# Kernel optimization log

Hardware: AMD Instinct MI355X
Metric: run time of the kernel (lower is better)

The kernel has to match this reference:

```python
import jax, jax.numpy as jnp
import numpy as np

V, D, H, B, M, T, PAD = 32000, 512, 3, 32, 512, 4, 1


def setup_inputs() -> dict:
    key = jax.random.key(0)
    ks = jax.random.split(key, 10)
    def emb_tables(k):
        t = 0.1 * jax.random.normal(k, (H + 1, V, D), jnp.float32)
        return t.at[:, PAD, :].set(0.0)  # padding_idx rows are zero
    C_enc = emb_tables(ks[0])
    C_dec = emb_tables(ks[1])
    gru_w_ih = 0.1 * jax.random.normal(ks[2], (3 * D, D), jnp.float32)
    gru_w_hh = 0.1 * jax.random.normal(ks[3], (3 * D, D), jnp.float32)
    gru_b_ih = jnp.zeros((3 * D,), jnp.float32)
    gru_b_hh = jnp.zeros((3 * D,), jnp.float32)
    W1_w = 0.1 * jax.random.normal(ks[4], (V, 2 * D), jnp.float32)
    W1_b = jnp.zeros((V,), jnp.float32)
    story = jax.random.randint(ks[5], (B, M, T), 0, V, jnp.int32)
    enc_query = jax.random.randint(ks[6], (B,), 0, V, jnp.int32)
    return {"story": story, "enc_query": enc_query, "C_enc": C_enc,
            "C_dec": C_dec, "gru_w_ih": gru_w_ih, "gru_w_hh": gru_w_hh,
            "gru_b_ih": gru_b_ih, "gru_b_hh": gru_b_hh, "W1_w": W1_w,
            "W1_b": W1_b}


def _mem_embed(table, story):
    # table [V, D], story [B, M, T] -> sum-pooled memory [B, M, D]
    return jnp.sum(table[story], axis=2)


def _forward(C_enc, C_dec, gru_w_ih, gru_w_hh, gru_b_ih, gru_b_hh,
             W1_w, W1_b, story, enc_query):
    # ---- EncoderMemNN.forward (eval mode, no unk_mask dropout) ----
    u = jnp.zeros((story.shape[0], D), C_enc.dtype)
    for hop in range(H):
        m_A = _mem_embed(C_enc[hop], story)            # [B, M, D]
        prob = jax.nn.softmax(jnp.einsum('bmd,bd->bm', m_A, u), axis=1)
        m_C = _mem_embed(C_enc[hop + 1], story)        # [B, M, D]
        u = u + jnp.einsum('bmd,bm->bd', m_C, prob)
    enc_hidden = u                                     # decoder_hidden[0]

    # ---- DecoderrMemNN.ptrMemDecoder: single GRU step ----
    x = C_dec[0][enc_query]                            # [B, D]
    gi = x @ gru_w_ih.T + gru_b_ih                     # [B, 3D]
    gh = enc_hidden @ gru_w_hh.T + gru_b_hh            # [B, 3D]
    i_r, i_z, i_n = jnp.split(gi, 3, axis=1)
    h_r, h_z, h_n = jnp.split(gh, 3, axis=1)
    r = jax.nn.sigmoid(i_r + h_r)
    z = jax.nn.sigmoid(i_z + h_z)
    n = jnp.tanh(i_n + r * h_n)
    hidden = (1.0 - z) * n + z * enc_hidden            # new GRU hidden [B, D]

    # ---- DecoderrMemNN.load_memory: m_story[h] = sum-pooled C_dec[h] ----
    m_story = [_mem_embed(C_dec[h], story) for h in range(H + 1)]

    # ---- multi-hop pointer attention ----
    u0 = hidden
    uk = hidden
    p_vocab = None
    for hop in range(H):
        prob_lg = jnp.einsum('bmd,bd->bm', m_story[hop], uk)   # [B, M]
        prob = jax.nn.softmax(prob_lg, axis=1)
        o_k = jnp.einsum('bmd,bm->bd', m_story[hop + 1], prob)  # [B, D]
        if hop == 0:
            p_vocab = jnp.concatenate([u0, o_k], axis=1) @ W1_w.T + W1_b
        uk = uk + o_k
    p_ptr = prob_lg                                    # logits from last hop
    return p_ptr, p_vocab, hidden[None]                # hidden [1, B, D]


def reference(story, enc_query, C_enc, C_dec, gru_w_ih, gru_w_hh,
              gru_b_ih, gru_b_hh, W1_w, W1_b):
    return _forward(C_enc, C_dec, gru_w_ih, gru_w_hh, gru_b_ih, gru_b_hh,
                    W1_w, W1_b, story, enc_query)
```

## Files before the change

kernel.cpp:

```cpp
#include <hip/hip_runtime.h>
#include <math.h>

#define DD 512
#define MM 512
#define BB 32
#define TT 4
#define VV 32000
#define BMD ((size_t)BB * MM * DD)

__global__ __launch_bounds__(256) void mega_pool(const float* __restrict__ C_enc,
                                                 const float* __restrict__ C_dec,
                                                 const int* __restrict__ story,
                                                 float* __restrict__ P) {
  int g = blockIdx.x;
  int tbl = g >> 12;
  int blk = g & 4095;
  int wave = (blk << 2) + (threadIdx.x >> 6);
  int lane = threadIdx.x & 63;
  const size_t VD = (size_t)VV * DD;
  const float* table = (tbl < 3) ? (C_enc + (size_t)(tbl + 1) * VD)
                                 : (C_dec + (size_t)(tbl - 3) * VD);
  const int* st = story + wave * TT;
  size_t r0 = (size_t)st[0] * DD, r1 = (size_t)st[1] * DD;
  size_t r2 = (size_t)st[2] * DD, r3 = (size_t)st[3] * DD;
  const float4* t4 = (const float4*)table;
  float4* p4 = (float4*)(P + (size_t)tbl * BMD + (size_t)wave * DD);
#pragma unroll
  for (int h = 0; h < 2; ++h) {
    int c = (h << 6) + lane;
    float4 a = t4[(r0 >> 2) + c];
    float4 b = t4[(r1 >> 2) + c];
    float4 cc = t4[(r2 >> 2) + c];
    float4 d = t4[(r3 >> 2) + c];
    float4 r;
    r.x = a.x + b.x + cc.x + d.x;
    r.y = a.y + b.y + cc.y + d.y;
    r.z = a.z + b.z + cc.z + d.z;
    r.w = a.w + b.w + cc.w + d.w;
    p4[c] = r;
  }
}

__global__ __launch_bounds__(256) void wsumA_kernel(const float* __restrict__ P,
                                                    const float* __restrict__ s,
                                                    float* __restrict__ partial) {
  __shared__ float wsh[MM];
  __shared__ float red[16];
  int b = blockIdx.x >> 3;
  int c = blockIdx.x & 7;
  int t = threadIdx.x;
  if (s) {
    float v0 = s[b * MM + t], v1 = s[b * MM + t + 256];
    float mx = fmaxf(v0, v1);
#pragma unroll
    for (int off = 32; off > 0; off >>= 1) mx = fmaxf(mx, __shfl_xor(mx, off));
    if ((t & 63) == 0) red[t >> 6] = mx;
    __syncthreads();
    mx = fmaxf(fmaxf(red[0], red[1]), fmaxf(red[2], red[3]));
    float e0 = expf(v0 - mx), e1 = expf(v1 - mx);
    float sm = e0 + e1;
#pragma unroll
    for (int off = 32; off > 0; off >>= 1) sm += __shfl_xor(sm, off);
    if ((t & 63) == 0) red[8 + (t >> 6)] = sm;
    __syncthreads();
    sm = red[8] + red[9] + red[10] + red[11];
    float inv = 1.0f / sm;
    wsh[t] = e0 * inv;
    wsh[t + 256] = e1 * inv;
    __syncthreads();
  }
  const float* Pb = P + ((size_t)b * MM + c * 64) * DD;
  float acc0 = 0.f, acc1 = 0.f;
  if (s) {
#pragma unroll 8
    for (int m = 0; m < 64; ++m) {
      float wm = wsh[c * 64 + m];
      acc0 += wm * Pb[m * DD + t];
      acc1 += wm * Pb[m * DD + t + 256];
    }
  } else {
#pragma unroll 8
    for (int m = 0; m < 64; ++m) {
      acc0 += Pb[m * DD + t];
      acc1 += Pb[m * DD + t + 256];
    }
    acc0 *= (1.0f / MM);
    acc1 *= (1.0f / MM);
  }
  float* pp = partial + (size_t)blockIdx.x * DD;
  pp[t] = acc0;
  pp[t + 256] = acc1;
}

__global__ void wsumB_kernel(const float* __restrict__ partial,
                             const float* __restrict__ prev,
                             float* __restrict__ uout) {
  int i = blockIdx.x * 256 + threadIdx.x;
  int b = i >> 9, d = i & 511;
  float acc = prev ? prev[i] : 0.f;
  const float* pp = partial + (size_t)b * 8 * DD + d;
#pragma unroll
  for (int c = 0; c < 8; ++c) acc += pp[c * DD];
  uout[i] = acc;
}

__global__ void wsumB2_kernel(const float* __restrict__ partial,
                              const float* __restrict__ hid,
                              float* __restrict__ uk, float* __restrict__ hc) {
  int i = blockIdx.x * 256 + threadIdx.x;
  int b = i >> 9, d = i & 511;
  float ov = 0.f;
  const float* pp = partial + (size_t)b * 8 * DD + d;
#pragma unroll
  for (int c = 0; c < 8; ++c) ov += pp[c * DD];
  float hv = hid[i];
  uk[i] = hv + ov;
  hc[b * 1024 + d] = hv;
  hc[b * 1024 + 512 + d] = ov;
}

__global__ __launch_bounds__(256) void dot_kernel(const float* __restrict__ P,
                                                  const float* __restrict__ u,
                                                  float* __restrict__ s) {
  int p = (blockIdx.x << 2) + (threadIdx.x >> 6);
  int lane = threadIdx.x & 63;
  int b = p >> 9;
  const float4* Pr = (const float4*)(P + (size_t)p * DD);
  const float4* ur = (const float4*)(u + (size_t)b * DD);
  float acc = 0.f;
#pragma unroll
  for (int h = 0; h < 2; ++h) {
    int c = (h << 6) + lane;
    float4 a = Pr[c];
    float4 q = ur[c];
    acc += a.x * q.x + a.y * q.y + a.z * q.z + a.w * q.w;
  }
#pragma unroll
  for (int off = 32; off > 0; off >>= 1) acc += __shfl_xor(acc, off);
  if (lane == 0) s[p] = acc;
}

__global__ __launch_bounds__(256) void matvec_kernel(const float* __restrict__ W,
                                                     const float* __restrict__ bias,
                                                     const float* __restrict__ vin,
                                                     const int* __restrict__ q,
                                                     const float* __restrict__ table,
                                                     float* __restrict__ out) {
  int idx = (blockIdx.x << 2) + (threadIdx.x >> 6);
  int lane = threadIdx.x & 63;
  int b = idx / 1536;
  int j = idx - b * 1536;
  const float* xb = vin ? (vin + (size_t)b * DD) : (table + (size_t)q[b] * DD);
  const float4* Wr = (const float4*)(W + (size_t)j * DD);
  const float4* xr = (const float4*)xb;
  float acc = 0.f;
#pragma unroll
  for (int h = 0; h < 2; ++h) {
    int c = (h << 6) + lane;
    float4 a = Wr[c];
    float4 qv = xr[c];
    acc += a.x * qv.x + a.y * qv.y + a.z * qv.z + a.w * qv.w;
  }
#pragma unroll
  for (int off = 32; off > 0; off >>= 1) acc += __shfl_xor(acc, off);
  if (lane == 0) out[idx] = acc + bias[j];
}

__global__ void gate_kernel(const float* __restrict__ gi, const float* __restrict__ gh,
                            const float* __restrict__ u, float* __restrict__ hidden,
                            float* __restrict__ out_h) {
  int i = blockIdx.x * 256 + threadIdx.x;
  int b = i >> 9, d = i & 511;
  const float* gib = gi + b * 1536;
  const float* ghb = gh + b * 1536;
  float i_r = gib[d], i_z = gib[d + 512], i_n = gib[d + 1024];
  float h_r = ghb[d], h_z = ghb[d + 512], h_n = ghb[d + 1024];
  float r = 1.f / (1.f + expf(-(i_r + h_r)));
  float z = 1.f / (1.f + expf(-(i_z + h_z)));
  float n = tanhf(i_n + r * h_n);
  float h = (1.f - z) * n + z * u[i];
  hidden[i] = h;
  out_h[i] = h;
}

__global__ __launch_bounds__(256) void pvocab_kernel(const float* __restrict__ Hcat,
                                                     const float* __restrict__ W1,
                                                     const float* __restrict__ W1b,
                                                     float* __restrict__ out) {
  __shared__ float As[32][36];
  __shared__ float Bs[32][68];
  int t = threadIdx.x;
  int v0 = blockIdx.x * 64;
  int tb = t >> 5;
  int tv = t & 31;
  int br = t >> 2;
  int bk = (t & 3) << 3;
  const float* Wp = W1 + (size_t)(v0 + br) * 1024 + bk;
  int ab = t >> 3;
  int ak = (t & 7) << 2;
  const float* Ap = Hcat + (size_t)ab * 1024 + ak;

  float acc[4][2] = {{0.f, 0.f}, {0.f, 0.f}, {0.f, 0.f}, {0.f, 0.f}};

  float4 aReg = *(const float4*)(Ap);
  float4 wReg0 = *(const float4*)(Wp);
  float4 wReg1 = *(const float4*)(Wp + 4);

  for (int k0 = 0; k0 < 1024; k0 += 32) {
    As[ak + 0][ab] = aReg.x; As[ak + 1][ab] = aReg.y;
    As[ak + 2][ab] = aReg.z; As[ak + 3][ab] = aReg.w;
    Bs[bk + 0][br] = wReg0.x; Bs[bk + 1][br] = wReg0.y;
    Bs[bk + 2][br] = wReg0.z; Bs[bk + 3][br] = wReg0.w;
    Bs[bk + 4][br] = wReg1.x; Bs[bk + 5][br] = wReg1.y;
    Bs[bk + 6][br] = wReg1.z; Bs[bk + 7][br] = wReg1.w;
    __syncthreads();
    if (k0 + 32 < 1024) {
      aReg = *(const float4*)(Ap + k0 + 32);
      wReg0 = *(const float4*)(Wp + k0 + 32);
      wReg1 = *(const float4*)(Wp + k0 + 36);
    }
#pragma unroll
    for (int k = 0; k < 32; ++k) {
      float2 bv = *(const float2*)&Bs[k][tv * 2];
      float4 av = *(const float4*)&As[k][tb * 4];
      acc[0][0] += av.x * bv.x; acc[0][1] += av.x * bv.y;
      acc[1][0] += av.y * bv.x; acc[1][1] += av.y * bv.y;
      acc[2][0] += av.z * bv.x; acc[2][1] += av.z * bv.y;
      acc[3][0] += av.w * bv.x; acc[3][1] += av.w * bv.y;
    }
    __syncthreads();
  }
  int v = v0 + tv * 2;
  float b0 = W1b[v], b1 = W1b[v + 1];
#pragma unroll
  for (int i = 0; i < 4; ++i) {
    float2 r;
    r.x = acc[i][0] + b0;
    r.y = acc[i][1] + b1;
    *(float2*)(out + (size_t)(tb * 4 + i) * VV + v) = r;
  }
}

extern "C" void kernel_launch(void* const* d_in, const int* in_sizes, int n_in,
                              void* d_out, int out_size, void* d_ws, size_t ws_size,
                              hipStream_t stream) {
  const int* story = (const int*)d_in[0];
  const int* q = (const int*)d_in[1];
  const float* C_enc = (const float*)d_in[2];
  const float* C_dec = (const float*)d_in[3];
  const float* W_ih = (const float*)d_in[4];
  const float* W_hh = (const float*)d_in[5];
  const float* b_ih = (const float*)d_in[6];
  const float* b_hh = (const float*)d_in[7];
  const float* W1 = (const float*)d_in[8];
  const float* W1b = (const float*)d_in[9];
  float* out = (float*)d_out;

  float* P = (float*)d_ws;
  float* u = P + 6 * BMD;
  float* s = u + BB * DD;
  float* part = s + BB * MM;
  float* gi = part + BB * 8 * DD;
  float* gh = gi + BB * 3 * DD;
  float* hid = gh + BB * 3 * DD;
  float* uk = hid + BB * DD;
  float* hc = uk + BB * DD;

  const float* P0 = P;
  const float* P1 = P + 1 * BMD;
  const float* P2 = P + 2 * BMD;
  const float* P3 = P + 3 * BMD;
  const float* P4 = P + 4 * BMD;
  const float* P5 = P + 5 * BMD;

  float* p_ptr_out = out;
  float* p_vocab_out = out + BB * MM;
  float* hid_out = out + BB * MM + (size_t)BB * VV;

  dim3 blk(256);
  const int dotGrid = BB * MM / 4;
  const int mvGrid = BB * 3 * DD / 4;
  const int ewGrid = BB * DD / 256;

  mega_pool<<<6 * 4096, blk, 0, stream>>>(C_enc, C_dec, story, P);

  wsumA_kernel<<<BB * 8, blk, 0, stream>>>(P0, nullptr, part);
  wsumB_kernel<<<ewGrid, blk, 0, stream>>>(part, nullptr, u);
  dot_kernel<<<dotGrid, blk, 0, stream>>>(P0, u, s);
  wsumA_kernel<<<BB * 8, blk, 0, stream>>>(P1, s, part);
  wsumB_kernel<<<ewGrid, blk, 0, stream>>>(part, u, u);
  dot_kernel<<<dotGrid, blk, 0, stream>>>(P1, u, s);
  wsumA_kernel<<<BB * 8, blk, 0, stream>>>(P2, s, part);
  wsumB_kernel<<<ewGrid, blk, 0, stream>>>(part, u, u);

  matvec_kernel<<<mvGrid, blk, 0, stream>>>(W_ih, b_ih, nullptr, q, C_dec, gi);
  matvec_kernel<<<mvGrid, blk, 0, stream>>>(W_hh, b_hh, u, nullptr, nullptr, gh);
  gate_kernel<<<ewGrid, blk, 0, stream>>>(gi, gh, u, hid, hid_out);

  dot_kernel<<<dotGrid, blk, 0, stream>>>(P3, hid, s);
  wsumA_kernel<<<BB * 8, blk, 0, stream>>>(P4, s, part);
  wsumB2_kernel<<<ewGrid, blk, 0, stream>>>(part, hid, uk, hc);
  dot_kernel<<<dotGrid, blk, 0, stream>>>(P4, uk, s);
  wsumA_kernel<<<BB * 8, blk, 0, stream>>>(P5, s, part);
  wsumB_kernel<<<ewGrid, blk, 0, stream>>>(part, uk, uk);
  dot_kernel<<<dotGrid, blk, 0, stream>>>(P5, uk, p_ptr_out);

  pvocab_kernel<<<VV / 64, blk, 0, stream>>>(hc, W1, W1b, p_vocab_out);
}
```

Measured before the change: 314.2 us.

## Fuse embedding gather-pooling into attention dot and weighted-sum kernels

Removes the upfront pooling kernel that materialized six pooled memory tensors in workspace, and instead gathers and sums embedding rows on the fly inside the dot-product and weighted-sum kernels. The weighted-sum kernel now splits each batch into 32 chunks of 16 memory slots, so the partial reductions sum over 32 partials. This avoids writing and re-reading about 200MB of pooled intermediates. In exchange each table is gathered twice (once for dot, once for weighted sum), with random-row access patterns.

```diff
diff --git a/kernel.cpp b/kernel.cpp
--- a/kernel.cpp
+++ b/kernel.cpp
@@ -6,48 +6,16 @@
 #define BB 32
 #define TT 4
 #define VV 32000
-#define BMD ((size_t)BB * MM * DD)
-
-__global__ __launch_bounds__(256) void mega_pool(const float* __restrict__ C_enc,
-                                                 const float* __restrict__ C_dec,
-                                                 const int* __restrict__ story,
-                                                 float* __restrict__ P) {
-  int g = blockIdx.x;
-  int tbl = g >> 12;
-  int blk = g & 4095;
-  int wave = (blk << 2) + (threadIdx.x >> 6);
-  int lane = threadIdx.x & 63;
-  const size_t VD = (size_t)VV * DD;
-  const float* table = (tbl < 3) ? (C_enc + (size_t)(tbl + 1) * VD)
-                                 : (C_dec + (size_t)(tbl - 3) * VD);
-  const int* st = story + wave * TT;
-  size_t r0 = (size_t)st[0] * DD, r1 = (size_t)st[1] * DD;
-  size_t r2 = (size_t)st[2] * DD, r3 = (size_t)st[3] * DD;
-  const float4* t4 = (const float4*)table;
-  float4* p4 = (float4*)(P + (size_t)tbl * BMD + (size_t)wave * DD);
-#pragma unroll
-  for (int h = 0; h < 2; ++h) {
-    int c = (h << 6) + lane;
-    float4 a = t4[(r0 >> 2) + c];
-    float4 b = t4[(r1 >> 2) + c];
-    float4 cc = t4[(r2 >> 2) + c];
-    float4 d = t4[(r3 >> 2) + c];
-    float4 r;
-    r.x = a.x + b.x + cc.x + d.x;
-    r.y = a.y + b.y + cc.y + d.y;
-    r.z = a.z + b.z + cc.z + d.z;
-    r.w = a.w + b.w + cc.w + d.w;
-    p4[c] = r;
-  }
-}
-
-__global__ __launch_bounds__(256) void wsumA_kernel(const float* __restrict__ P,
-                                                    const float* __restrict__ s,
-                                                    float* __restrict__ partial) {
-  __shared__ float wsh[MM];
+
+__global__ __launch_bounds__(256) void poolwsum_kernel(const float* __restrict__ table,
+                                                       const int* __restrict__ story,
+                                                       const float* __restrict__ s,
+                                                       float* __restrict__ partial) {
+  __shared__ float wsh[16];
+  __shared__ int rows[64];
   __shared__ float red[16];
-  int b = blockIdx.x >> 3;
-  int c = blockIdx.x & 7;
+  int b = blockIdx.x >> 5;
+  int c = blockIdx.x & 31;
   int t = threadIdx.x;
   if (s) {
     float v0 = s[b * MM + t], v1 = s[b * MM + t + 256];
@@ -65,27 +33,19 @@
     __syncthreads();
     sm = red[8] + red[9] + red[10] + red[11];
     float inv = 1.0f / sm;
-    wsh[t] = e0 * inv;
-    wsh[t + 256] = e1 * inv;
-    __syncthreads();
-  }
-  const float* Pb = P + ((size_t)b * MM + c * 64) * DD;
+    if (t < 16) wsh[t] = expf(s[b * MM + c * 16 + t] - mx) * inv;
+  } else {
+    if (t < 16) wsh[t] = 1.0f / MM;
+  }
+  if (t < 64) rows[t] = story[((b << 9) + (c << 4)) * TT + t];
+  __syncthreads();
   float acc0 = 0.f, acc1 = 0.f;
-  if (s) {
 #pragma unroll 8
-    for (int m = 0; m < 64; ++m) {
-      float wm = wsh[c * 64 + m];
-      acc0 += wm * Pb[m * DD + t];
-      acc1 += wm * Pb[m * DD + t + 256];
-    }
-  } else {
-#pragma unroll 8
-    for (int m = 0; m < 64; ++m) {
-      acc0 += Pb[m * DD + t];
-      acc1 += Pb[m * DD + t + 256];
-    }
-    acc0 *= (1.0f / MM);
-    acc1 *= (1.0f / MM);
+  for (int i = 0; i < 64; ++i) {
+    const float* r = table + (size_t)rows[i] * DD;
+    float wm = wsh[i >> 2];
+    acc0 += wm * r[t];
+    acc1 += wm * r[t + 256];
   }
   float* pp = partial + (size_t)blockIdx.x * DD;
   pp[t] = acc0;
@@ -98,9 +58,9 @@
   int i = blockIdx.x * 256 + threadIdx.x;
   int b = i >> 9, d = i & 511;
   float acc = prev ? prev[i] : 0.f;
-  const float* pp = partial + (size_t)b * 8 * DD + d;
-#pragma unroll
-  for (int c = 0; c < 8; ++c) acc += pp[c * DD];
+  const float* pp = partial + (size_t)b * 32 * DD + d;
+#pragma unroll
+  for (int c = 0; c < 32; ++c) acc += pp[c * DD];
   uout[i] = acc;
 }
 
@@ -110,34 +70,44 @@
   int i = blockIdx.x * 256 + threadIdx.x;
   int b = i >> 9, d = i & 511;
   float ov = 0.f;
-  const float* pp = partial + (size_t)b * 8 * DD + d;
-#pragma unroll
-  for (int c = 0; c < 8; ++c) ov += pp[c * DD];
+  const float* pp = partial + (size_t)b * 32 * DD + d;
+#pragma unroll
+  for (int c = 0; c < 32; ++c) ov += pp[c * DD];
   float hv = hid[i];
   uk[i] = hv + ov;
   hc[b * 1024 + d] = hv;
   hc[b * 1024 + 512 + d] = ov;
 }
 
-__global__ __launch_bounds__(256) void dot_kernel(const float* __restrict__ P,
-                                                  const float* __restrict__ u,
-                                                  float* __restrict__ s) {
-  int p = (blockIdx.x << 2) + (threadIdx.x >> 6);
+__global__ __launch_bounds__(256) void pooldot_kernel(const float* __restrict__ table,
+                                                      const int* __restrict__ story,
+                                                      const float* __restrict__ u,
+                                                      float* __restrict__ s) {
+  int wave = (blockIdx.x << 2) + (threadIdx.x >> 6);
   int lane = threadIdx.x & 63;
-  int b = p >> 9;
-  const float4* Pr = (const float4*)(P + (size_t)p * DD);
+  int b = wave >> 9;
+  const int* st = story + wave * TT;
+  size_t r0 = (size_t)st[0] * DD, r1 = (size_t)st[1] * DD;
+  size_t r2 = (size_t)st[2] * DD, r3 = (size_t)st[3] * DD;
+  const float4* t4 = (const float4*)table;
   const float4* ur = (const float4*)(u + (size_t)b * DD);
   float acc = 0.f;
 #pragma unroll
   for (int h = 0; h < 2; ++h) {
     int c = (h << 6) + lane;
-    float4 a = Pr[c];
+    float4 a = t4[(r0 >> 2) + c];
+    float4 bb = t4[(r1 >> 2) + c];
+    float4 cc = t4[(r2 >> 2) + c];
+    float4 d = t4[(r3 >> 2) + c];
     float4 q = ur[c];
-    acc += a.x * q.x + a.y * q.y + a.z * q.z + a.w * q.w;
+    acc += (a.x + bb.x + cc.x + d.x) * q.x;
+    acc += (a.y + bb.y + cc.y + d.y) * q.y;
+    acc += (a.z + bb.z + cc.z + d.z) * q.z;
+    acc += (a.w + bb.w + cc.w + d.w) * q.w;
   }
 #pragma unroll
   for (int off = 32; off > 0; off >>= 1) acc += __shfl_xor(acc, off);
-  if (lane == 0) s[p] = acc;
+  if (lane == 0) s[wave] = acc;
 }
 
 __global__ __launch_bounds__(256) void matvec_kernel(const float* __restrict__ W,
@@ -256,54 +226,53 @@
   const float* W1b = (const float*)d_in[9];
   float* out = (float*)d_out;
 
-  float* P = (float*)d_ws;
-  float* u = P + 6 * BMD;
+  const size_t VD = (size_t)VV * DD;
+  const float* C1 = C_enc + 1 * VD;
+  const float* C2 = C_enc + 2 * VD;
+  const float* C3 = C_enc + 3 * VD;
+  const float* D0 = C_dec + 0 * VD;
+  const float* D1 = C_dec + 1 * VD;
+  const float* D2 = C_dec + 2 * VD;
+
+  float* part = (float*)d_ws;
+  float* u = part + (size_t)BB * 32 * DD;
   float* s = u + BB * DD;
-  float* part = s + BB * MM;
-  float* gi = part + BB * 8 * DD;
+  float* gi = s + BB * MM;
   float* gh = gi + BB * 3 * DD;
   float* hid = gh + BB * 3 * DD;
   float* uk = hid + BB * DD;
   float* hc = uk + BB * DD;
 
-  const float* P0 = P;
-  const float* P1 = P + 1 * BMD;
-  const float* P2 = P + 2 * BMD;
-  const float* P3 = P + 3 * BMD;
-  const float* P4 = P + 4 * BMD;
-  const float* P5 = P + 5 * BMD;
-
   float* p_ptr_out = out;
   float* p_vocab_out = out + BB * MM;
   float* hid_out = out + BB * MM + (size_t)BB * VV;
 
   dim3 blk(256);
-  const int dotGrid = BB * MM / 4;
+  const int pwGrid = BB * 32;
+  const int pdGrid = BB * MM / 4;
   const int mvGrid = BB * 3 * DD / 4;
   const int ewGrid = BB * DD / 256;
 
-  mega_pool<<<6 * 4096, blk, 0, stream>>>(C_enc, C_dec, story, P);
-
-  wsumA_kernel<<<BB * 8, blk, 0, stream>>>(P0, nullptr, part);
+  poolwsum_kernel<<<pwGrid, blk, 0, stream>>>(C1, story, nullptr, part);
   wsumB_kernel<<<ewGrid, blk, 0, stream>>>(part, nullptr, u);
-  dot_kernel<<<dotGrid, blk, 0, stream>>>(P0, u, s);
-  wsumA_kernel<<<BB * 8, blk, 0, stream>>>(P1, s, part);
+  pooldot_kernel<<<pdGrid, blk, 0, stream>>>(C1, story, u, s);
+  poolwsum_kernel<<<pwGrid, blk, 0, stream>>>(C2, story, s, part);
   wsumB_kernel<<<ewGrid, blk, 0, stream>>>(part, u, u);
-  dot_kernel<<<dotGrid, blk, 0, stream>>>(P1, u, s);
-  wsumA_kernel<<<BB * 8, blk, 0, stream>>>(P2, s, part);
+  pooldot_kernel<<<pdGrid, blk, 0, stream>>>(C2, story, u, s);
+  poolwsum_kernel<<<pwGrid, blk, 0, stream>>>(C3, story, s, part);
   wsumB_kernel<<<ewGrid, blk, 0, stream>>>(part, u, u);
 
   matvec_kernel<<<mvGrid, blk, 0, stream>>>(W_ih, b_ih, nullptr, q, C_dec, gi);
   matvec_kernel<<<mvGrid, blk, 0, stream>>>(W_hh, b_hh, u, nullptr, nullptr, gh);
   gate_kernel<<<ewGrid, blk, 0, stream>>>(gi, gh, u, hid, hid_out);
 
-  dot_kernel<<<dotGrid, blk, 0, stream>>>(P3, hid, s);
-  wsumA_kernel<<<BB * 8, blk, 0, stream>>>(P4, s, part);
+  pooldot_kernel<<<pdGrid, blk, 0, stream>>>(D0, story, hid, s);
+  poolwsum_kernel<<<pwGrid, blk, 0, stream>>>(D1, story, s, part);
   wsumB2_kernel<<<ewGrid, blk, 0, stream>>>(part, hid, uk, hc);
-  dot_kernel<<<dotGrid, blk, 0, stream>>>(P4, uk, s);
-  wsumA_kernel<<<BB * 8, blk, 0, stream>>>(P5, s, part);
+  pooldot_kernel<<<pdGrid, blk, 0, stream>>>(D1, story, uk, s);
+  poolwsum_kernel<<<pwGrid, blk, 0, stream>>>(D2, story, s, part);
   wsumB_kernel<<<ewGrid, blk, 0, stream>>>(part, uk, uk);
-  dot_kernel<<<dotGrid, blk, 0, stream>>>(P5, uk, p_ptr_out);
+  pooldot_kernel<<<pdGrid, blk, 0, stream>>>(D2, story, uk, p_ptr_out);
 
   pvocab_kernel<<<VV / 64, blk, 0, stream>>>(hc, W1, W1b, p_vocab_out);
 }
```

Measured after the change: 297.7 us. 5.3% less time.
